# Optimization experiments

Measured on AMD Instinct MI355X. Metric: run time of the kernel, lower is better.

## Reference

```python
import jax, jax.numpy as jnp
import numpy as np
from math import factorial

ORDER = 5
CUTOFF_HZ = 45e9
FS = 160e9
BATCH, T = 16, 1048576


def _bessel_coeffs(n, cutoff, fs):
    """Digital lowpass Bessel filter (norm='mag'), replicating scipy.signal.bessel.
    Pure numpy: reverse Bessel polynomial poles -> magnitude normalization
    (|H(j*1)| = 1/sqrt(2)) via bisection -> frequency prewarp -> bilinear transform.
    """
    # reverse Bessel polynomial theta_n(s): coeff of s^k
    c = np.array([factorial(2 * n - k) / (2.0 ** (n - k) * factorial(k) * factorial(n - k))
                  for k in range(n + 1)], dtype=np.float64)
    poles0 = np.roots(c[::-1])  # analog prototype poles (unnormalized)

    def mag_at_1(alpha):
        p = alpha * poles0
        k = np.real(np.prod(-p))  # unity DC gain numerator
        return np.abs(k / np.prod(1j - p))

    # bisection (log scale) for -3 dB magnitude at w = 1  (scipy norm='mag')
    lo, hi = 1e-3, 1e3
    target = 1.0 / np.sqrt(2.0)
    for _ in range(200):
        mid = np.sqrt(lo * hi)
        if mag_at_1(mid) < target:
            lo = mid
        else:
            hi = mid
    alpha = np.sqrt(lo * hi)

    warped = 2.0 * fs * np.tan(np.pi * cutoff / fs)  # bilinear prewarp
    p = alpha * poles0 * warped                      # analog poles at desired cutoff
    k = np.real(np.prod(-p))                         # unity DC gain
    fs2 = 2.0 * fs
    pd = (fs2 + p) / (fs2 - p)                       # bilinear: digital poles
    kd = k / np.real(np.prod(fs2 - p))
    b = kd * np.real(np.poly(-np.ones(n)))           # n zeros at z = -1
    a = np.real(np.poly(pd))
    return b, a


def _lfilter(x, b, a):
    """IIR filter, direct form II transposed; x: [B, T], b/a: [order+1]."""
    b = b / a[0]
    a = a / a[0]
    n = a.shape[0] - 1
    bsz = x.shape[0]

    def step(z, xt):  # z: [B, n] delay state, xt: [B]
        y = b[0] * xt + z[:, 0]
        z_new = xt[:, None] * b[1:] - y[:, None] * a[1:]
        z_new = z_new.at[:, :-1].add(z[:, 1:])
        return z_new, y

    z0 = jnp.zeros((bsz, n), dtype=x.dtype)
    _, ys = jax.lax.scan(step, z0, x.T)  # scan over time axis -> ys: [T, B]
    return ys.T


def setup_inputs() -> dict:
    key = jax.random.key(0)
    x = jax.random.normal(key, (BATCH, T), dtype=jnp.float32)
    b_np, a_np = _bessel_coeffs(ORDER, CUTOFF_HZ, FS)
    return {
        "x": x,
        "b": jnp.asarray(b_np, dtype=jnp.float32),
        "a": jnp.asarray(a_np, dtype=jnp.float32),
    }


def reference(x, b, a):
    xmax = jnp.max(jnp.abs(x))
    return xmax * _lfilter(x / xmax, b, a)
```

## Files before the change

### kernel.cpp

```cpp
#include <hip/hip_runtime.h>


#define K_TAPS 20
#define OPT 8
#define BLOCK 256
#define OPB (BLOCK * OPT)
#define T_LEN 1048576
#define BATCH 16
#define TILES_PER_ROW (T_LEN / OPB)
#define NW (OPT + K_TAPS)
#define NV (NW / 4)

typedef float fx4 __attribute__((ext_vector_type(4)));

__global__ __launch_bounds__(BLOCK, 8) void bessel_fused(
    const float* __restrict__ x, const float* __restrict__ bcoef,
    const float* __restrict__ acoef, float* __restrict__ y) {
    const int bid  = blockIdx.x;
    const int row  = bid >> 9;
    const int tile = bid & (TILES_PER_ROW - 1);
    const int G    = tile * OPB + (int)threadIdx.x * OPT;
    const float* __restrict__ xr = x + (size_t)row * T_LEN;
    float* __restrict__ yr       = y + (size_t)row * T_LEN;

    __shared__ float hsh[K_TAPS];

    fx4 v[NV];
    if (G >= K_TAPS) {
        const fx4* src = (const fx4*)(xr + (G - K_TAPS));
#pragma unroll
        for (int i = 0; i < NV; ++i) v[i] = src[i];
    } else {
        float tmp[NW];
#pragma unroll
        for (int i = 0; i < NW; ++i) {
            int gi = G - K_TAPS + i;
            tmp[i] = (gi >= 0) ? xr[gi] : 0.0f;
        }
#pragma unroll
        for (int i = 0; i < NV; ++i)
            v[i] = (fx4){tmp[4*i], tmp[4*i+1], tmp[4*i+2], tmp[4*i+3]};
    }
    __builtin_amdgcn_sched_barrier(0);

    if (threadIdx.x == 0) {
        float bb[6], aa[6];
        float inv = 1.0f / acoef[0];
#pragma unroll
        for (int i = 0; i < 6; ++i) { bb[i] = bcoef[i] * inv; aa[i] = acoef[i] * inv; }
        float z0 = 0.f, z1 = 0.f, z2 = 0.f, z3 = 0.f, z4 = 0.f;
#pragma unroll
        for (int t = 0; t < K_TAPS; ++t) {
            float xt = (t == 0) ? 1.0f : 0.0f;
            float yv = fmaf(bb[0], xt, z0);
            z0 = fmaf(bb[1], xt, z1) - aa[1] * yv;
            z1 = fmaf(bb[2], xt, z2) - aa[2] * yv;
            z2 = fmaf(bb[3], xt, z3) - aa[3] * yv;
            z3 = fmaf(bb[4], xt, z4) - aa[4] * yv;
            z4 = bb[5] * xt - aa[5] * yv;
            hsh[t] = yv;
        }
    }
    __syncthreads();

    float hs[K_TAPS];
#pragma unroll
    for (int k = 0; k < K_TAPS; ++k)
        hs[k] = __int_as_float(__builtin_amdgcn_readfirstlane(__float_as_int(hsh[k])));

    float acc[OPT];
#pragma unroll
    for (int j = 0; j < OPT; ++j) acc[j] = 0.0f;
#pragma unroll
    for (int k = 0; k < K_TAPS; ++k) {
#pragma unroll
        for (int j = 0; j < OPT; ++j) {
            const int i = K_TAPS + j - k;
            acc[j] = fmaf(hs[k], v[i >> 2][i & 3], acc[j]);
        }
    }

    fx4* oy = (fx4*)(yr + G);
#pragma unroll
    for (int q = 0; q < OPT / 4; ++q) {
        fx4 o = {acc[4*q], acc[4*q+1], acc[4*q+2], acc[4*q+3]};
        oy[q] = o;
    }
}

extern "C" void kernel_launch(void* const* d_in, const int* in_sizes, int n_in,
                              void* d_out, int out_size, void* d_ws, size_t ws_size,
                              hipStream_t stream) {
    const float* x = (const float*)d_in[0];
    const float* b = (const float*)d_in[1];
    const float* a = (const float*)d_in[2];
    float* y = (float*)d_out;

    hipLaunchKernelGGL(bessel_fused, dim3(BATCH * TILES_PER_ROW), dim3(BLOCK), 0,
                       stream, x, b, a, y);
}
```

Before: 25.78 us.

## Process four tiles per block with double-buffered loads and fewer FIR taps

Cuts the grid to 2048 blocks, each handling four tiles. The next tile's input is loaded into a second register buffer while the current one is computed and stored, and the impulse response is built once per block instead of once per tile. The FIR truncation also drops from 20 to 16 taps, which removes multiply-adds and halo loads but slightly increases truncation error against the IIR reference. Holding two buffers raises register pressure, and fewer blocks means less parallelism for hiding latency.

```diff
diff --git a/kernel.cpp b/kernel.cpp
--- a/kernel.cpp
+++ b/kernel.cpp
@@ -1,13 +1,15 @@
 #include <hip/hip_runtime.h>
 
 
-#define K_TAPS 20
+#define K_TAPS 16
 #define OPT 8
 #define BLOCK 256
 #define OPB (BLOCK * OPT)
 #define T_LEN 1048576
 #define BATCH 16
 #define TILES_PER_ROW (T_LEN / OPB)
+#define NTILES (BATCH * TILES_PER_ROW)
+#define NBLOCKS 2048
 #define NW (OPT + K_TAPS)
 #define NV (NW / 4)
 
@@ -16,34 +18,54 @@
 __global__ __launch_bounds__(BLOCK, 8) void bessel_fused(
     const float* __restrict__ x, const float* __restrict__ bcoef,
     const float* __restrict__ acoef, float* __restrict__ y) {
-    const int bid  = blockIdx.x;
-    const int row  = bid >> 9;
-    const int tile = bid & (TILES_PER_ROW - 1);
-    const int G    = tile * OPB + (int)threadIdx.x * OPT;
-    const float* __restrict__ xr = x + (size_t)row * T_LEN;
-    float* __restrict__ yr       = y + (size_t)row * T_LEN;
+    const int tid = (int)threadIdx.x;
+    const int t0  = (int)blockIdx.x;
+    __shared__ float hsh[K_TAPS];
+    float hs[K_TAPS];
+    fx4 A[NV], B[NV];
 
-    __shared__ float hsh[K_TAPS];
+    auto loadw = [&](fx4 (&v)[NV], int tt) {
+        const int row = tt >> 9;
+        const int G   = (tt & (TILES_PER_ROW - 1)) * OPB + tid * OPT;
+        const float* __restrict__ xr = x + (size_t)row * T_LEN;
+        if (G >= K_TAPS) {
+            const fx4* src = (const fx4*)(xr + (G - K_TAPS));
+#pragma unroll
+            for (int i = 0; i < NV; ++i) v[i] = src[i];
+        } else {
+#pragma unroll
+            for (int i = 0; i < NV; ++i)
+#pragma unroll
+                for (int c = 0; c < 4; ++c) {
+                    int gi = G - K_TAPS + 4 * i + c;
+                    v[i][c] = (gi >= 0) ? xr[gi] : 0.0f;
+                }
+        }
+    };
 
-    fx4 v[NV];
-    if (G >= K_TAPS) {
-        const fx4* src = (const fx4*)(xr + (G - K_TAPS));
+    auto compute_store = [&](fx4 (&v)[NV], int tt) {
+        const int row = tt >> 9;
+        const int G   = (tt & (TILES_PER_ROW - 1)) * OPB + tid * OPT;
+        fx4* oy = (fx4*)(y + (size_t)row * T_LEN + G);
 #pragma unroll
-        for (int i = 0; i < NV; ++i) v[i] = src[i];
-    } else {
-        float tmp[NW];
+        for (int half = 0; half < 2; ++half) {
+            float acc[4] = {0.f, 0.f, 0.f, 0.f};
 #pragma unroll
-        for (int i = 0; i < NW; ++i) {
-            int gi = G - K_TAPS + i;
-            tmp[i] = (gi >= 0) ? xr[gi] : 0.0f;
+            for (int k = 0; k < K_TAPS; ++k) {
+#pragma unroll
+                for (int j = 0; j < 4; ++j) {
+                    const int i = K_TAPS + 4 * half + j - k;
+                    acc[j] = fmaf(hs[k], v[i >> 2][i & 3], acc[j]);
+                }
+            }
+            fx4 o = {acc[0], acc[1], acc[2], acc[3]};
+            oy[half] = o;
         }
-#pragma unroll
-        for (int i = 0; i < NV; ++i)
-            v[i] = (fx4){tmp[4*i], tmp[4*i+1], tmp[4*i+2], tmp[4*i+3]};
-    }
+    };
+
+    loadw(A, t0);
     __builtin_amdgcn_sched_barrier(0);
-
-    if (threadIdx.x == 0) {
+    if (tid == 0) {
         float bb[6], aa[6];
         float inv = 1.0f / acoef[0];
 #pragma unroll
@@ -62,30 +84,23 @@
         }
     }
     __syncthreads();
-
-    float hs[K_TAPS];
 #pragma unroll
     for (int k = 0; k < K_TAPS; ++k)
         hs[k] = __int_as_float(__builtin_amdgcn_readfirstlane(__float_as_int(hsh[k])));
 
-    float acc[OPT];
-#pragma unroll
-    for (int j = 0; j < OPT; ++j) acc[j] = 0.0f;
-#pragma unroll
-    for (int k = 0; k < K_TAPS; ++k) {
-#pragma unroll
-        for (int j = 0; j < OPT; ++j) {
-            const int i = K_TAPS + j - k;
-            acc[j] = fmaf(hs[k], v[i >> 2][i & 3], acc[j]);
-        }
-    }
+    loadw(B, t0 + NBLOCKS);
+    __builtin_amdgcn_sched_barrier(0);
+    compute_store(A, t0);
 
-    fx4* oy = (fx4*)(yr + G);
-#pragma unroll
-    for (int q = 0; q < OPT / 4; ++q) {
-        fx4 o = {acc[4*q], acc[4*q+1], acc[4*q+2], acc[4*q+3]};
-        oy[q] = o;
-    }
+    loadw(A, t0 + 2 * NBLOCKS);
+    __builtin_amdgcn_sched_barrier(0);
+    compute_store(B, t0 + NBLOCKS);
+
+    loadw(B, t0 + 3 * NBLOCKS);
+    __builtin_amdgcn_sched_barrier(0);
+    compute_store(A, t0 + 2 * NBLOCKS);
+
+    compute_store(B, t0 + 3 * NBLOCKS);
 }
 
 extern "C" void kernel_launch(void* const* d_in, const int* in_sizes, int n_in,
@@ -96,6 +111,6 @@
     const float* a = (const float*)d_in[2];
     float* y = (float*)d_out;
 
-    hipLaunchKernelGGL(bessel_fused, dim3(BATCH * TILES_PER_ROW), dim3(BLOCK), 0,
+    hipLaunchKernelGGL(bessel_fused, dim3(NBLOCKS), dim3(BLOCK), 0,
                        stream, x, b, a, y);
 }
```

Measured after the change: 40.28 us. +56.2%, slower.
